# Kernel tuning notes

Measured on AMD Instinct MI355X. Metric: run time of the kernel, lower is better.

Reference implementation:

```python
import jax, jax.numpy as jnp
import numpy as np

N_NODES = 100000
N_EDGES = 1000000
D_IN = 64
D_HID = 64
D_OUT = 64


def setup_inputs() -> dict:
    key = jax.random.key(0)
    ks = jax.random.split(key, 8)
    x = jax.random.normal(ks[0], (N_NODES, D_IN), dtype=jnp.float32)
    edge_index = jax.random.randint(ks[1], (2, N_EDGES), 0, N_NODES, dtype=jnp.int64)
    s = 1.0 / np.sqrt(D_IN)
    # SAGEConv layer 1: lin_l (applied to aggregated neighbors, with bias), lin_r (root, no bias)
    W1l = jax.random.uniform(ks[2], (D_HID, D_IN), jnp.float32, -s, s)
    b1l = jnp.zeros((D_HID,), jnp.float32)
    W1r = jax.random.uniform(ks[3], (D_HID, D_IN), jnp.float32, -s, s)
    s2 = 1.0 / np.sqrt(D_HID)
    W2l = jax.random.uniform(ks[4], (D_OUT, D_HID), jnp.float32, -s2, s2)
    b2l = jnp.zeros((D_OUT,), jnp.float32)
    W2r = jax.random.uniform(ks[5], (D_OUT, D_HID), jnp.float32, -s2, s2)
    return {"x": x, "edge_index": edge_index,
            "W1l": W1l, "b1l": b1l, "W1r": W1r,
            "W2l": W2l, "b2l": b2l, "W2r": W2r}


def _sage_conv(x, src, dst, Wl, bl, Wr):
    # mean-aggregate neighbor features (messages flow src -> dst)
    msg_sum = jax.ops.segment_sum(x[src], dst, num_segments=N_NODES)  # [N, d]
    deg = jax.ops.segment_sum(jnp.ones((src.shape[0],), x.dtype), dst, num_segments=N_NODES)
    agg = msg_sum / jnp.maximum(deg, 1.0)[:, None]
    return agg @ Wl.T + bl + x @ Wr.T


def reference(x, edge_index, W1l, b1l, W1r, W2l, b2l, W2r):
    src, dst = edge_index[0], edge_index[1]
    h = _sage_conv(x, src, dst, W1l, b1l, W1r)
    h = jax.nn.relu(h)
    # dropout is identity in eval mode
    out = _sage_conv(h, src, dst, W2l, b2l, W2r)
    return out
```

## Files before the change

### kernel.cpp

```cpp
#include <hip/hip_runtime.h>

#define D 64
#define BK_SHIFT 8
#define BK_MASK 255
#define SEGCAP 4096
#define ESLICE 4096

typedef __attribute__((ext_vector_type(8))) short short8;
typedef __attribute__((ext_vector_type(4))) float floatx4;

__device__ __forceinline__ ushort f2bf(float f) {
    unsigned u = __float_as_uint(f);
    u += 0x7fffu + ((u >> 16) & 1u);
    return (ushort)(u >> 16);
}
__device__ __forceinline__ float bf2f(ushort h) {
    return __int_as_float(((unsigned)h) << 16);
}

__global__ void cast_bkcount_kernel(const float* __restrict__ x, ushort* __restrict__ xh,
                                    const int* __restrict__ ei, int* __restrict__ bkcnt,
                                    int* __restrict__ scnt,
                                    int n4, int E, int B, int castb) {
    int bid = blockIdx.x;
    int tid = threadIdx.x;
    if (bid < castb) {
        int i = bid * 256 + tid;
        if (i >= n4) return;
        float4 v = ((const float4*)x)[i];
        ushort4 r;
        r.x = f2bf(v.x); r.y = f2bf(v.y); r.z = f2bf(v.z); r.w = f2bf(v.w);
        ((ushort4*)xh)[i] = r;
        return;
    }
    __shared__ int h[512];
    h[tid] = 0; h[tid + 256] = 0;
    __syncthreads();
    int slice = bid - castb;
    int e0 = slice * ESLICE;
#pragma unroll 4
    for (int it = 0; it < ESLICE / 256; ++it) {
        int e = e0 + it * 256 + tid;
        if (e < E) atomicAdd(&h[ei[E + e] >> BK_SHIFT], 1);
    }
    __syncthreads();
    scnt[slice * 512 + tid] = h[tid];
    scnt[slice * 512 + 256 + tid] = h[tid + 256];
    if (tid < B && h[tid]) atomicAdd(&bkcnt[tid], h[tid]);
    int t2 = tid + 256;
    if (t2 < B && h[t2]) atomicAdd(&bkcnt[t2], h[t2]);
}

__global__ void route_kernel(const int* __restrict__ ei, const int* __restrict__ scnt,
                             const int* __restrict__ bkcnt, int* __restrict__ bkoff,
                             int* __restrict__ bkbeg, int* __restrict__ bucketed,
                             int E, int B) {
    __shared__ int h[512];
    __shared__ int gb[512];
    __shared__ int wsum[4];
    int tid = threadIdx.x;
    int slice = blockIdx.x;
    int a = (2 * tid < B) ? bkcnt[2 * tid] : 0;
    int b = (2 * tid + 1 < B) ? bkcnt[2 * tid + 1] : 0;
    int s = a + b;
    int lane = tid & 63, w = tid >> 6;
    int p = s;
#pragma unroll
    for (int o = 1; o < 64; o <<= 1) {
        int u = __shfl_up(p, o, 64);
        if (lane >= o) p += u;
    }
    if (lane == 63) wsum[w] = p;
    __syncthreads();
    int base = 0;
    for (int ww = 0; ww < w; ++ww) base += wsum[ww];
    int excl = base + p - s;
    gb[2 * tid] = excl;
    gb[2 * tid + 1] = excl + a;
    if (slice == 0) {
        bkbeg[2 * tid] = excl;
        bkbeg[2 * tid + 1] = excl + a;
        if (tid == 255) bkbeg[512] = excl + s;
    }
    __syncthreads();
    int c0 = scnt[slice * 512 + tid];
    int c1 = scnt[slice * 512 + 256 + tid];
    if (c0) gb[tid] += atomicAdd(&bkoff[tid], c0);
    if (c1) gb[tid + 256] += atomicAdd(&bkoff[tid + 256], c1);
    h[tid] = 0; h[tid + 256] = 0;
    __syncthreads();
    int e0 = slice * ESLICE;
#pragma unroll 4
    for (int it = 0; it < ESLICE / 256; ++it) {
        int e = e0 + it * 256 + tid;
        if (e < E) {
            int dst = ei[E + e];
            int key = dst >> BK_SHIFT;
            int src = ei[e];
            int r = atomicAdd(&h[key], 1);
            bucketed[gb[key] + r] = (src << BK_SHIFT) | (dst & BK_MASK);
        }
    }
}

__global__ void csr_kernel(const int* __restrict__ bucketed, const int* __restrict__ bkbeg,
                           int* __restrict__ srclist, int* __restrict__ beg,
                           int* __restrict__ cnt, int* __restrict__ hist, int N) {
    __shared__ int lcnt[256];
    __shared__ int lbeg[256];
    __shared__ int seg[SEGCAP];
    __shared__ int wsum[4];
    __shared__ int lh[64];
    int k = blockIdx.x;
    int tid = threadIdx.x;
    int nd0 = k << BK_SHIFT;
    int nn = min(256, N - nd0);
    int ebeg = bkbeg[k], eend = bkbeg[k + 1];
    int ecnt = eend - ebeg;
    lcnt[tid] = 0;
    if (tid < 64) lh[tid] = 0;
    __syncthreads();
    for (int e = ebeg + tid; e < eend; e += 256)
        atomicAdd(&lcnt[bucketed[e] & BK_MASK], 1);
    __syncthreads();
    int c = lcnt[tid];
    int lane = tid & 63, w = tid >> 6;
    int p = c;
#pragma unroll
    for (int o = 1; o < 64; o <<= 1) {
        int u = __shfl_up(p, o, 64);
        if (lane >= o) p += u;
    }
    if (lane == 63) wsum[w] = p;
    __syncthreads();
    int base = 0;
    for (int ww = 0; ww < w; ++ww) base += wsum[ww];
    int excl = base + p - c;
    lbeg[tid] = excl;
    lcnt[tid] = 0;
    __syncthreads();
    if (ecnt <= SEGCAP) {
        for (int e = ebeg + tid; e < eend; e += 256) {
            int v = bucketed[e];
            int key = v & BK_MASK;
            int pos = lbeg[key] + atomicAdd(&lcnt[key], 1);
            seg[pos] = v >> BK_SHIFT;
        }
        __syncthreads();
        for (int i = tid; i < ecnt; i += 256)
            srclist[ebeg + i] = seg[i];
    } else {
        for (int e = ebeg + tid; e < eend; e += 256) {
            int v = bucketed[e];
            int key = v & BK_MASK;
            int pos = lbeg[key] + atomicAdd(&lcnt[key], 1);
            srclist[ebeg + pos] = v >> BK_SHIFT;
        }
    }
    __syncthreads();
    if (tid < nn) {
        int dg = lcnt[tid];
        cnt[nd0 + tid] = dg;
        beg[nd0 + tid] = ebeg + lbeg[tid];
        atomicAdd(&lh[dg < 63 ? dg : 63], 1);
    }
    __syncthreads();
    if (tid < 64 && lh[tid]) atomicAdd(&hist[tid], lh[tid]);
}

__global__ void scatter_kernel(const int* __restrict__ cnt, const int* __restrict__ hist,
                               int* __restrict__ bincur0, int* __restrict__ perm, int N) {
    __shared__ int lh[64];
    __shared__ int lbase[64];
    __shared__ int sbase[64];
    int tid = threadIdx.x;
    if (tid < 64) {
        lh[tid] = 0;
        int c = hist[tid];
        int p = c;
#pragma unroll
        for (int o = 1; o < 64; o <<= 1) {
            int u = __shfl_up(p, o, 64);
            if (tid >= o) p += u;
        }
        sbase[tid] = N - p;
    }
    __syncthreads();
    int i = blockIdx.x * blockDim.x + tid;
    int bin = 0, slot = 0;
    if (i < N) {
        int c = cnt[i];
        bin = c < 63 ? c : 63;
        slot = atomicAdd(&lh[bin], 1);
    }
    __syncthreads();
    if (tid < 64 && lh[tid] > 0) lbase[tid] = sbase[tid] + atomicAdd(&bincur0[tid], lh[tid]);
    __syncthreads();
    if (i < N) perm[lbase[bin] + slot] = i;
}


__global__ void __launch_bounds__(256, 3) sage_kernel(
    const ushort* __restrict__ inh,
    const int* __restrict__ perm,
    const int* __restrict__ beg_, const int* __restrict__ cnt_,
    const int* __restrict__ srclist,
    const float* __restrict__ Wl, const float* __restrict__ bl,
    const float* __restrict__ Wr,
    float* __restrict__ out_f32,
    ushort* __restrict__ out_bf,
    int N, int relu) {
    __shared__ short8 fL[8][64];
    __shared__ short8 fR[8][64];
    int tid = threadIdx.x;
    int lane = tid & 63;
    {
        int c = tid >> 6;
        int n = lane & 15;
        int q = lane >> 4;
#pragma unroll
        for (int s = 0; s < 2; ++s) {
            const float* pl = Wl + (c * 16 + n) * D + s * 32 + q * 8;
            const float* pr = Wr + (c * 16 + n) * D + s * 32 + q * 8;
            short8 vl, vr;
#pragma unroll
            for (int j = 0; j < 8; ++j) {
                vl[j] = (short)f2bf(pl[j]);
                vr[j] = (short)f2bf(pr[j]);
            }
            fL[c * 2 + s][lane] = vl;
            fR[c * 2 + s][lane] = vr;
        }
    }
    __syncthreads();

    int m = lane & 15;
    int q = lane >> 4;
    float b0 = bl[m], b1 = bl[16 + m], b2 = bl[32 + m], b3 = bl[48 + m];
    int gwave   = blockIdx.x * 4 + (tid >> 6);
    int nwaves  = gridDim.x * 4;
    int ngroups = (N + 15) >> 4;

    for (int g = gwave; g < ngroups; g += nwaves) {
        int base = g * 16;
        bool nv = (base + m) < N;
        int node = nv ? perm[base + m] : 0;
        int beg = nv ? beg_[node] : 0;
        int deg = nv ? cnt_[node] : 0;

        int md = deg;
        md = max(md, __shfl_xor(md, 1, 64));
        md = max(md, __shfl_xor(md, 2, 64));
        md = max(md, __shfl_xor(md, 4, 64));
        md = max(md, __shfl_xor(md, 8, 64));

        float f0[8], f1[8];
#pragma unroll
        for (int u = 0; u < 8; ++u) { f0[u] = 0.f; f1[u] = 0.f; }

        for (int j = 0; j < md; j += 4) {
            int si0, si1, si2, si3;
            {
                int j0 = j,     i0 = beg + ((j0 < deg) ? j0 : 0);
                int j1 = j + 1, i1 = beg + ((j1 < deg) ? j1 : 0);
                int j2 = j + 2, i2 = beg + ((j2 < deg) ? j2 : 0);
                int j3 = j + 3, i3 = beg + ((j3 < deg) ? j3 : 0);
                si0 = srclist[i0]; si1 = srclist[i1];
                si2 = srclist[i2]; si3 = srclist[i3];
            }
            const ushort* rp0 = inh + (size_t)si0 * D;
            const ushort* rp1 = inh + (size_t)si1 * D;
            const ushort* rp2 = inh + (size_t)si2 * D;
            const ushort* rp3 = inh + (size_t)si3 * D;
            short8 lo0 = *(const short8*)(rp0 + q * 8);
            short8 hi0 = *(const short8*)(rp0 + 32 + q * 8);
            short8 lo1 = *(const short8*)(rp1 + q * 8);
            short8 hi1 = *(const short8*)(rp1 + 32 + q * 8);
            short8 lo2 = *(const short8*)(rp2 + q * 8);
            short8 hi2 = *(const short8*)(rp2 + 32 + q * 8);
            short8 lo3 = *(const short8*)(rp3 + q * 8);
            short8 hi3 = *(const short8*)(rp3 + 32 + q * 8);
            float m0 = (j     < deg) ? 1.f : 0.f;
            float m1 = (j + 1 < deg) ? 1.f : 0.f;
            float m2 = (j + 2 < deg) ? 1.f : 0.f;
            float m3 = (j + 3 < deg) ? 1.f : 0.f;
#pragma unroll
            for (int u = 0; u < 8; ++u) {
                f0[u] = fmaf(m0, bf2f((ushort)lo0[u]), f0[u]);
                f1[u] = fmaf(m0, bf2f((ushort)hi0[u]), f1[u]);
                f0[u] = fmaf(m1, bf2f((ushort)lo1[u]), f0[u]);
                f1[u] = fmaf(m1, bf2f((ushort)hi1[u]), f1[u]);
                f0[u] = fmaf(m2, bf2f((ushort)lo2[u]), f0[u]);
                f1[u] = fmaf(m2, bf2f((ushort)hi2[u]), f1[u]);
                f0[u] = fmaf(m3, bf2f((ushort)lo3[u]), f0[u]);
                f1[u] = fmaf(m3, bf2f((ushort)hi3[u]), f1[u]);
            }
        }

        float scale = (deg > 0) ? 1.0f / (float)deg : 0.0f;
        short8 a0, a1;
#pragma unroll
        for (int u = 0; u < 8; ++u) {
            a0[u] = (short)f2bf(f0[u] * scale);
            a1[u] = (short)f2bf(f1[u] * scale);
        }

        const ushort* rr = inh + (size_t)node * D;
        short8 r0 = *(const short8*)(rr + q * 8);
        short8 r1 = *(const short8*)(rr + 32 + q * 8);

        int on0 = __shfl(node, q * 4 + 0, 64);
        int on1 = __shfl(node, q * 4 + 1, 64);
        int on2 = __shfl(node, q * 4 + 2, 64);
        int on3 = __shfl(node, q * 4 + 3, 64);
        bool v0 = (base + q * 4 + 0) < N;
        bool v1 = (base + q * 4 + 1) < N;
        bool v2 = (base + q * 4 + 2) < N;
        bool v3 = (base + q * 4 + 3) < N;

#pragma unroll
        for (int c = 0; c < 4; ++c) {
            float bc = (c == 0) ? b0 : (c == 1) ? b1 : (c == 2) ? b2 : b3;
            floatx4 acc = {bc, bc, bc, bc};
            acc = __builtin_amdgcn_mfma_f32_16x16x32_bf16(a0, fL[c * 2 + 0][lane], acc, 0, 0, 0);
            acc = __builtin_amdgcn_mfma_f32_16x16x32_bf16(a1, fL[c * 2 + 1][lane], acc, 0, 0, 0);
            acc = __builtin_amdgcn_mfma_f32_16x16x32_bf16(r0, fR[c * 2 + 0][lane], acc, 0, 0, 0);
            acc = __builtin_amdgcn_mfma_f32_16x16x32_bf16(r1, fR[c * 2 + 1][lane], acc, 0, 0, 0);
#pragma unroll
            for (int r = 0; r < 4; ++r) {
                float v = acc[r];
                if (relu) v = fmaxf(v, 0.f);
                int onr = (r == 0) ? on0 : (r == 1) ? on1 : (r == 2) ? on2 : on3;
                bool vr = (r == 0) ? v0 : (r == 1) ? v1 : (r == 2) ? v2 : v3;
                if (vr) {
                    size_t off = (size_t)onr * D + c * 16 + m;
                    if (out_bf) out_bf[off] = f2bf(v);
                    else        out_f32[off] = v;
                }
            }
        }
    }
}

extern "C" void kernel_launch(void* const* d_in, const int* in_sizes, int n_in,
                              void* d_out, int out_size, void* d_ws, size_t ws_size,
                              hipStream_t stream) {
    const float* x   = (const float*)d_in[0];
    const int*   ei  = (const int*)d_in[1];
    const float* W1l = (const float*)d_in[2];
    const float* b1l = (const float*)d_in[3];
    const float* W1r = (const float*)d_in[4];
    const float* W2l = (const float*)d_in[5];
    const float* b2l = (const float*)d_in[6];
    const float* W2r = (const float*)d_in[7];
    float* out = (float*)d_out;

    int N = in_sizes[0] / D;
    int E = in_sizes[1] / 2;
    int B = (N + BK_MASK) >> BK_SHIFT;
    int eslices = (E + ESLICE - 1) / ESLICE;

    char* ws = (char*)d_ws;
    ushort* xh = (ushort*)ws;
    ushort* hh = xh + (size_t)N * D;
    int*   bucketed = (int*)hh;
    int*   srclist  = (int*)(ws + (size_t)2 * N * D * 2);
    int*   beg      = srclist + E + 64;
    int*   cnt      = beg + N;
    int*   perm     = cnt + N;
    int*   hist     = perm + N;
    int*   bincur0  = hist + 64;
    int*   bkcnt    = bincur0 + 64;
    int*   bkoff    = bkcnt + 512;
    int*   bkbeg    = bkoff + 512;
    int*   scnt     = bkbeg + 513;

    (void)hipMemsetAsync(hist, 0, (64 + 64 + 512 + 512) * sizeof(int), stream);

    int n4 = N * D / 4;
    int castb = (n4 + 255) / 256;
    cast_bkcount_kernel<<<castb + eslices, 256, 0, stream>>>(x, xh, ei, bkcnt, scnt,
                                                             n4, E, B, castb);
    route_kernel<<<eslices, 256, 0, stream>>>(ei, scnt, bkcnt, bkoff, bkbeg,
                                              bucketed, E, B);
    csr_kernel<<<B, 256, 0, stream>>>(bucketed, bkbeg, srclist, beg, cnt, hist, N);
    int nblocks = (N + 255) / 256;
    scatter_kernel<<<nblocks, 256, 0, stream>>>(cnt, hist, bincur0, perm, N);

    int ngroups = (N + 15) / 16;
    int sblocks = (ngroups + 3) / 4;
    sage_kernel<<<sblocks, 256, 0, stream>>>(xh, perm, beg, cnt, srclist,
                                             W1l, b1l, W1r, nullptr, hh, N, 1);
    sage_kernel<<<sblocks, 256, 0, stream>>>(hh, perm, beg, cnt, srclist,
                                             W2l, b2l, W2r, out, nullptr, N, 0);
}
```

Baseline: 209.2 us.

## Fold degree-sort permutation into CSR kernel with per-bucket local ordering

```diff
diff --git a/kernel.cpp b/kernel.cpp
--- a/kernel.cpp
+++ b/kernel.cpp
@@ -4,7 +4,7 @@
 #define BK_SHIFT 8
 #define BK_MASK 255
 #define SEGCAP 4096
-#define ESLICE 4096
+#define ESLICE 2048
 
 typedef __attribute__((ext_vector_type(8))) short short8;
 typedef __attribute__((ext_vector_type(4))) float floatx4;
@@ -105,12 +105,13 @@
 
 __global__ void csr_kernel(const int* __restrict__ bucketed, const int* __restrict__ bkbeg,
                            int* __restrict__ srclist, int* __restrict__ beg,
-                           int* __restrict__ cnt, int* __restrict__ hist, int N) {
+                           int* __restrict__ cnt, int* __restrict__ perm, int N) {
     __shared__ int lcnt[256];
     __shared__ int lbeg[256];
     __shared__ int seg[SEGCAP];
     __shared__ int wsum[4];
     __shared__ int lh[64];
+    __shared__ int sfx[64];
     int k = blockIdx.x;
     int tid = threadIdx.x;
     int nd0 = k << BK_SHIFT;
@@ -118,7 +119,6 @@
     int ebeg = bkbeg[k], eend = bkbeg[k + 1];
     int ecnt = eend - ebeg;
     lcnt[tid] = 0;
-    if (tid < 64) lh[tid] = 0;
     __syncthreads();
     for (int e = ebeg + tid; e < eend; e += 256)
         atomicAdd(&lcnt[bucketed[e] & BK_MASK], 1);
@@ -158,45 +158,33 @@
         }
     }
     __syncthreads();
+    int dg = 0;
     if (tid < nn) {
-        int dg = lcnt[tid];
+        dg = lcnt[tid];
         cnt[nd0 + tid] = dg;
         beg[nd0 + tid] = ebeg + lbeg[tid];
-        atomicAdd(&lh[dg < 63 ? dg : 63], 1);
-    }
-    __syncthreads();
-    if (tid < 64 && lh[tid]) atomicAdd(&hist[tid], lh[tid]);
-}
-
-__global__ void scatter_kernel(const int* __restrict__ cnt, const int* __restrict__ hist,
-                               int* __restrict__ bincur0, int* __restrict__ perm, int N) {
-    __shared__ int lh[64];
-    __shared__ int lbase[64];
-    __shared__ int sbase[64];
-    int tid = threadIdx.x;
+    }
+    int bin = dg < 63 ? dg : 63;
+    if (tid < 64) lh[tid] = 0;
+    __syncthreads();
+    if (tid < nn) atomicAdd(&lh[bin], 1);
+    __syncthreads();
     if (tid < 64) {
+        int cc = lh[tid];
+        int pp = cc;
+#pragma unroll
+        for (int o = 1; o < 64; o <<= 1) {
+            int u = __shfl_down(pp, o, 64);
+            if (tid + o < 64) pp += u;
+        }
+        sfx[tid] = pp - cc;
         lh[tid] = 0;
-        int c = hist[tid];
-        int p = c;
-#pragma unroll
-        for (int o = 1; o < 64; o <<= 1) {
-            int u = __shfl_up(p, o, 64);
-            if (tid >= o) p += u;
-        }
-        sbase[tid] = N - p;
-    }
-    __syncthreads();
-    int i = blockIdx.x * blockDim.x + tid;
-    int bin = 0, slot = 0;
-    if (i < N) {
-        int c = cnt[i];
-        bin = c < 63 ? c : 63;
-        slot = atomicAdd(&lh[bin], 1);
-    }
-    __syncthreads();
-    if (tid < 64 && lh[tid] > 0) lbase[tid] = sbase[tid] + atomicAdd(&bincur0[tid], lh[tid]);
-    __syncthreads();
-    if (i < N) perm[lbase[bin] + slot] = i;
+    }
+    __syncthreads();
+    if (tid < nn) {
+        int rank = sfx[bin] + atomicAdd(&lh[bin], 1);
+        perm[nd0 + rank] = nd0 + tid;
+    }
 }
 
 
@@ -368,14 +356,12 @@
     int*   beg      = srclist + E + 64;
     int*   cnt      = beg + N;
     int*   perm     = cnt + N;
-    int*   hist     = perm + N;
-    int*   bincur0  = hist + 64;
-    int*   bkcnt    = bincur0 + 64;
+    int*   bkcnt    = perm + N;
     int*   bkoff    = bkcnt + 512;
     int*   bkbeg    = bkoff + 512;
     int*   scnt     = bkbeg + 513;
 
-    (void)hipMemsetAsync(hist, 0, (64 + 64 + 512 + 512) * sizeof(int), stream);
+    (void)hipMemsetAsync(bkcnt, 0, (512 + 512) * sizeof(int), stream);
 
     int n4 = N * D / 4;
     int castb = (n4 + 255) / 256;
@@ -383,9 +369,7 @@
                                                              n4, E, B, castb);
     route_kernel<<<eslices, 256, 0, stream>>>(ei, scnt, bkcnt, bkoff, bkbeg,
                                               bucketed, E, B);
-    csr_kernel<<<B, 256, 0, stream>>>(bucketed, bkbeg, srclist, beg, cnt, hist, N);
-    int nblocks = (N + 255) / 256;
-    scatter_kernel<<<nblocks, 256, 0, stream>>>(cnt, hist, bincur0, perm, N);
+    csr_kernel<<<B, 256, 0, stream>>>(bucketed, bkbeg, srclist, beg, cnt, perm, N);
 
     int ngroups = (N + 15) / 16;
     int sblocks = (ngroups + 3) / 4;
```

Result: slower. 225.1 us (+7.6%).
